# Kernel optimization log

Measured on AMD Instinct MI355X. Metric: run time of the kernel, lower is better.

## Reference

```python
import jax, jax.numpy as jnp
import numpy as np

N_NODES = 50000
N_EDGES = 800000
IN_CH = 128
MEAN_SIZE = 128
VAR_SIZE = 128


def setup_inputs() -> dict:
    key = jax.random.key(0)
    k_x, k_e, k_wm, k_wv = jax.random.split(key, 4)
    x = jax.random.normal(k_x, (N_NODES, IN_CH), dtype=jnp.float32)
    edge_index = jax.random.randint(k_e, (2, N_EDGES), 0, N_NODES, dtype=jnp.int32)
    # torch Linear(2*C, M, bias=False) weight has shape [M, 2*C]
    s = 1.0 / np.sqrt(2 * IN_CH)
    w_mean = jax.random.uniform(k_wm, (MEAN_SIZE, 2 * IN_CH), jnp.float32, -s, s)
    w_var = jax.random.uniform(k_wv, (VAR_SIZE, 2 * IN_CH), jnp.float32, -s, s)
    return {"x": x, "edge_index": edge_index, "w_mean": w_mean, "w_var": w_var}


def reference(x, edge_index, w_mean, w_var):
    row, col = edge_index[0], edge_index[1]
    x_row = x[row]  # [E, C]
    x_col = x[col]  # [E, C]
    # cat([x_row, x_col], 1) @ W.T  ==  x_row @ W[:, :C].T + x_col @ W[:, C:].T
    C = x.shape[1]
    maps_mean = jnp.einsum('ec,mc->em', x_row, w_mean[:, :C]) + \
                jnp.einsum('ec,mc->em', x_col, w_mean[:, C:])
    maps_var = jnp.einsum('ec,vc->ev', x_row, w_var[:, :C]) + \
               jnp.einsum('ec,vc->ev', x_col, w_var[:, C:])
    return (maps_mean, maps_var)
```

## Files before the change

kernel.cpp:

```cpp
#include <hip/hip_runtime.h>
#include <hip/hip_bf16.h>

#define NODES 50000
#define EDGES 800000
#define CH 128
#define NCOL 512
#define MPAD 50048
#define QROWS 64
#define EPW 4

typedef __attribute__((ext_vector_type(8))) __bf16 bf16x8;
typedef __attribute__((ext_vector_type(4))) float f32x4;
typedef __attribute__((ext_vector_type(2))) float f32x2;
typedef unsigned long long u64;

static __device__ __forceinline__ unsigned short f2bf(float f) {
    union { float f; unsigned u; } v; v.f = f;
    unsigned r = v.u + 0x7FFFu + ((v.u >> 16) & 1u);
    return (unsigned short)(r >> 16);
}

__global__ void k_cvt_x(const float* __restrict__ x, unsigned short* __restrict__ xb) {
    int i = blockIdx.x * blockDim.x + threadIdx.x;
    if (i >= MPAD * CH / 4) return;
    int base = i << 2;
    unsigned short s0 = 0, s1 = 0, s2 = 0, s3 = 0;
    if (base < NODES * CH) {
        const f32x4 v = *reinterpret_cast<const f32x4*>(x + base);
        s0 = f2bf(v[0]); s1 = f2bf(v[1]); s2 = f2bf(v[2]); s3 = f2bf(v[3]);
    }
    u64 p = (u64)s0 | ((u64)s1 << 16) | ((u64)s2 << 32) | ((u64)s3 << 48);
    *reinterpret_cast<u64*>(xb + base) = p;
}

__global__ void k_pack_w(const float* __restrict__ wm, const float* __restrict__ wv,
                         unsigned short* __restrict__ wb) {
    int i = blockIdx.x * blockDim.x + threadIdx.x;
    if (i >= NCOL * CH) return;
    int n = i >> 7, k = i & 127;
    float v;
    if (n < 128)      v = wm[n * 256 + k];
    else if (n < 256) v = wm[(n - 128) * 256 + 128 + k];
    else if (n < 384) v = wv[(n - 256) * 256 + k];
    else              v = wv[(n - 384) * 256 + 128 + k];
    wb[i] = f2bf(v);
}

__global__ __launch_bounds__(256) void k_gemmq(const unsigned short* __restrict__ xb,
                                               const unsigned short* __restrict__ wb,
                                               char* __restrict__ qt,
                                               float* __restrict__ sc) {
    __shared__ float sM[2][2][QROWS];
    __shared__ __align__(16) char sQ[QROWS][NCOL];
    const int lane = threadIdx.x & 63;
    const int wave = threadIdx.x >> 6;
    const int rowbase = blockIdx.x * QROWS;
    const int lr = lane & 15;
    const int kg = lane >> 4;

    f32x4 acc[4][8] = {};
#pragma unroll
    for (int ks = 0; ks < 4; ++ks) {
        const int k = ks * 32 + kg * 8;
        bf16x8 af[4], bfr[8];
#pragma unroll
        for (int a = 0; a < 4; ++a)
            af[a] = *reinterpret_cast<const bf16x8*>(xb + (size_t)(rowbase + a * 16 + lr) * CH + k);
#pragma unroll
        for (int b = 0; b < 8; ++b)
            bfr[b] = *reinterpret_cast<const bf16x8*>(wb + (size_t)(wave * 128 + lr * 8 + b) * CH + k);
#pragma unroll
        for (int a = 0; a < 4; ++a)
#pragma unroll
            for (int b = 0; b < 8; ++b)
                acc[a][b] = __builtin_amdgcn_mfma_f32_16x16x32_bf16(af[a], bfr[b], acc[a][b], 0, 0, 0);
    }

    const int crow = (lane >> 4) * 4;
    const int ccol = lane & 15;
    const int half = wave >> 1;

    float m[4][4];
#pragma unroll
    for (int a = 0; a < 4; ++a)
#pragma unroll
        for (int j = 0; j < 4; ++j) {
            float mm = 0.f;
#pragma unroll
            for (int b = 0; b < 8; ++b) mm = fmaxf(mm, fabsf(acc[a][b][j]));
            m[a][j] = mm;
        }
#pragma unroll
    for (int off = 1; off < 16; off <<= 1)
#pragma unroll
        for (int a = 0; a < 4; ++a)
#pragma unroll
            for (int j = 0; j < 4; ++j)
                m[a][j] = fmaxf(m[a][j], __shfl_xor(m[a][j], off, 16));
    if (ccol == 0)
#pragma unroll
        for (int a = 0; a < 4; ++a)
#pragma unroll
            for (int j = 0; j < 4; ++j)
                sM[half][wave & 1][a * 16 + crow + j] = m[a][j];
    __syncthreads();

#pragma unroll
    for (int a = 0; a < 4; ++a)
#pragma unroll
        for (int j = 0; j < 4; ++j) {
            const int row = a * 16 + crow + j;
            const float rm = fmaxf(sM[half][0][row], sM[half][1][row]);
            const float inv = (rm > 1e-20f) ? 127.0f / rm : 0.0f;
            u64 pk = 0;
#pragma unroll
            for (int b = 0; b < 8; ++b) {
                int q = __float2int_rn(acc[a][b][j] * inv);
                q = max(-127, min(127, q));
                pk |= (u64)((unsigned)q & 0xFFu) << (8 * b);
            }
            *reinterpret_cast<u64*>(&sQ[row][wave * 128 + ccol * 8]) = pk;
        }
    if (threadIdx.x < 2 * QROWS) {
        const int h = threadIdx.x >> 6, row = threadIdx.x & 63;
        const float rm = fmaxf(sM[h][0][row], sM[h][1][row]);
        sc[(size_t)(rowbase + row) * 2 + h] = (rm > 1e-20f) ? rm * (1.0f / 127.0f) : 1.0f;
    }
    __syncthreads();

#pragma unroll
    for (int t = 0; t < 8; ++t) {
        const int off = t * 4096 + threadIdx.x * 16;
        f32x4 v = *reinterpret_cast<const f32x4*>(&sQ[0][0] + off);
        *reinterpret_cast<f32x4*>(qt + (size_t)rowbase * NCOL + off) = v;
    }
}

__global__ __launch_bounds__(256) void k_edges_m(const int* __restrict__ ei,
                                                 const char* __restrict__ qt,
                                                 const float* __restrict__ sc,
                                                 float* __restrict__ out) {
    const int wave = threadIdx.x >> 6;
    const int lane = threadIdx.x & 63;
    const int es = lane >> 5;
    const int j = lane & 31;
    const int ebase = (blockIdx.x * 4 + wave) * (2 * EPW);

    int rr[EPW], cc[EPW];
#pragma unroll
    for (int i = 0; i < EPW; ++i) {
        int e = ebase + 2 * i + es;
        rr[i] = ei[e];
        cc[i] = ei[EDGES + e];
    }
    int am[EPW], av[EPW], bm[EPW], bv[EPW];
    f32x2 sr[EPW], scl[EPW];
#pragma unroll
    for (int i = 0; i < EPW; ++i) {
        const char* qr = qt + (size_t)rr[i] * NCOL;
        const char* qc = qt + (size_t)cc[i] * NCOL;
        am[i] = *reinterpret_cast<const int*>(qr + j * 4);
        av[i] = *reinterpret_cast<const int*>(qr + 256 + j * 4);
        bm[i] = *reinterpret_cast<const int*>(qc + 128 + j * 4);
        bv[i] = *reinterpret_cast<const int*>(qc + 384 + j * 4);
        sr[i]  = *reinterpret_cast<const f32x2*>(sc + (size_t)rr[i] * 2);
        scl[i] = *reinterpret_cast<const f32x2*>(sc + (size_t)cc[i] * 2);
    }
#pragma unroll
    for (int i = 0; i < EPW; ++i) {
        const int e = ebase + 2 * i + es;
        f32x4 sm_, sv_;
#pragma unroll
        for (int k = 0; k < 4; ++k) {
            const int sh = 24 - 8 * k;
            sm_[k] = sr[i][0] * (float)((am[i] << sh) >> 24)
                   + scl[i][0] * (float)((bm[i] << sh) >> 24);
            sv_[k] = sr[i][1] * (float)((av[i] << sh) >> 24)
                   + scl[i][1] * (float)((bv[i] << sh) >> 24);
        }
        __builtin_nontemporal_store(sm_,
            reinterpret_cast<f32x4*>(out + (size_t)e * 128 + j * 4));
        __builtin_nontemporal_store(sv_,
            reinterpret_cast<f32x4*>(out + (size_t)EDGES * 128 + (size_t)e * 128 + j * 4));
    }
}

__global__ void k_naive(const float* __restrict__ x, const int* __restrict__ ei,
                        const float* __restrict__ wm, const float* __restrict__ wv,
                        float* __restrict__ out) {
    __shared__ float xs[256];
    int e = blockIdx.x;
    int t = threadIdx.x;
    int r = ei[e], c = ei[EDGES + e];
    xs[t] = (t < 128) ? x[(size_t)r * 128 + t] : x[(size_t)c * 128 + (t - 128)];
    __syncthreads();
    const float* w = (t < 128) ? (wm + (size_t)t * 256) : (wv + (size_t)(t - 128) * 256);
    float acc = 0.f;
#pragma unroll 8
    for (int k = 0; k < 256; ++k) acc = fmaf(xs[k], w[k], acc);
    size_t ooff = (t < 128) ? ((size_t)e * 128 + t)
                            : ((size_t)EDGES * 128 + (size_t)e * 128 + (t - 128));
    out[ooff] = acc;
}

extern "C" void kernel_launch(void* const* d_in, const int* in_sizes, int n_in,
                              void* d_out, int out_size, void* d_ws, size_t ws_size,
                              hipStream_t stream) {
    const float* x  = (const float*)d_in[0];
    const int*   ei = (const int*)d_in[1];
    const float* wm = (const float*)d_in[2];
    const float* wv = (const float*)d_in[3];
    float* out = (float*)d_out;

    const size_t xb_b = (size_t)MPAD * CH * 2;
    const size_t wb_b = (size_t)NCOL * CH * 2;
    const size_t qt_b = (size_t)MPAD * NCOL;
    const size_t sc_b = (size_t)MPAD * 2 * 4;

    if (ws_size < xb_b + wb_b + qt_b + sc_b) {
        k_naive<<<EDGES, 256, 0, stream>>>(x, ei, wm, wv, out);
        return;
    }

    unsigned short* xb = (unsigned short*)d_ws;
    unsigned short* wb = (unsigned short*)((char*)d_ws + xb_b);
    char*           qt = (char*)d_ws + xb_b + wb_b;
    float*          sc = (float*)((char*)d_ws + xb_b + wb_b + qt_b);

    k_cvt_x<<<(MPAD * CH / 4 + 255) / 256, 256, 0, stream>>>(x, xb);
    k_pack_w<<<(NCOL * CH + 255) / 256, 256, 0, stream>>>(wm, wv, wb);
    k_gemmq<<<MPAD / QROWS, 256, 0, stream>>>(xb, wb, qt, sc);
    k_edges_m<<<EDGES / (4 * 2 * EPW), 256, 0, stream>>>(ei, qt, sc, out);
}
```

Baseline: 226.5 us.

## Group edges by source node via CSR build to reuse row projections

Builds a CSR grouping of edges by source node (histogram, single-block scan, atomic scatter) and adds an edge kernel with one wave per node. The row-side projection is loaded once per node and reused across its edges, while the column side is still gathered per edge. In exchange it adds five extra launches, a serial single-block scan, atomics, scattered output writes in nondeterministic edge order, and load imbalance from varying node degree.

```diff
diff --git a/kernel.cpp b/kernel.cpp
--- a/kernel.cpp
+++ b/kernel.cpp
@@ -136,6 +136,92 @@
     }
 }
 
+__global__ void k_zero(unsigned* __restrict__ cnt) {
+    int i = blockIdx.x * blockDim.x + threadIdx.x;
+    if (i < NODES) cnt[i] = 0;
+}
+__global__ void k_histn(const int* __restrict__ ei, unsigned* __restrict__ cnt) {
+    int e = blockIdx.x * 256 + threadIdx.x;
+    atomicAdd(&cnt[ei[e]], 1u);
+}
+__global__ __launch_bounds__(256) void k_scan(const unsigned* __restrict__ cnt,
+                                              unsigned* __restrict__ rowptr,
+                                              unsigned* __restrict__ cursor) {
+    __shared__ unsigned part[256];
+    const int t = threadIdx.x;
+    const int per = (NODES + 255) / 256;
+    const int lo = t * per, hi = min(NODES, lo + per);
+    unsigned s = 0;
+    for (int i = lo; i < hi; ++i) s += cnt[i];
+    part[t] = s;
+    __syncthreads();
+    for (int off = 1; off < 256; off <<= 1) {
+        unsigned x = (t >= off) ? part[t - off] : 0;
+        __syncthreads();
+        part[t] += x;
+        __syncthreads();
+    }
+    unsigned run = part[t] - s;
+    for (int i = lo; i < hi; ++i) { rowptr[i] = run; cursor[i] = run; run += cnt[i]; }
+}
+__global__ void k_scatter(const int* __restrict__ ei, unsigned* __restrict__ cursor,
+                          u64* __restrict__ packed) {
+    int e = blockIdx.x * 256 + threadIdx.x;
+    int r = ei[e];
+    unsigned c = (unsigned)ei[EDGES + e];
+    unsigned pos = atomicAdd(&cursor[r], 1u);
+    packed[pos] = (u64)c | ((u64)e << 32);
+}
+
+__global__ __launch_bounds__(256) void k_edges_csr(const unsigned* __restrict__ rowptr,
+                                                   const unsigned* __restrict__ cnt,
+                                                   const u64* __restrict__ packed,
+                                                   const char* __restrict__ qt,
+                                                   const float* __restrict__ sc,
+                                                   float* __restrict__ out) {
+    const int wave = threadIdx.x >> 6;
+    const int node = blockIdx.x * 4 + wave;
+    const int lane = threadIdx.x & 63;
+    const int half = lane >> 5;
+    const int j = lane & 31;
+    const unsigned start = rowptr[node];
+    const unsigned deg = cnt[node];
+    const int ar = *reinterpret_cast<const int*>(qt + (size_t)node * NCOL + half * 256 + j * 4);
+    const float s_r = sc[(size_t)node * 2 + half];
+    const size_t ob = (size_t)half * ((size_t)EDGES * 128) + (size_t)j * 4;
+
+    for (unsigned k0 = 0; k0 < deg; k0 += 4) {
+        const int n = (int)min(4u, deg - k0);
+        u64 pk[4];
+#pragma unroll
+        for (int i = 0; i < 4; ++i)
+            if (i < n) pk[i] = packed[start + k0 + i];
+        int ac[4]; float s_c[4]; unsigned ee[4];
+#pragma unroll
+        for (int i = 0; i < 4; ++i)
+            if (i < n) {
+                const unsigned c = (unsigned)(pk[i] & 0xFFFFFFFFu);
+                ee[i] = (unsigned)(pk[i] >> 32);
+                ac[i] = *reinterpret_cast<const int*>(
+                    qt + (size_t)c * NCOL + 128 + half * 256 + j * 4);
+                s_c[i] = sc[(size_t)c * 2 + half];
+            }
+#pragma unroll
+        for (int i = 0; i < 4; ++i)
+            if (i < n) {
+                f32x4 v;
+#pragma unroll
+                for (int k = 0; k < 4; ++k) {
+                    const int sh = 24 - 8 * k;
+                    v[k] = s_r * (float)((ar << sh) >> 24)
+                         + s_c[i] * (float)((ac[i] << sh) >> 24);
+                }
+                __builtin_nontemporal_store(v,
+                    reinterpret_cast<f32x4*>(out + ob + (size_t)ee[i] * 128));
+            }
+    }
+}
+
 __global__ __launch_bounds__(256) void k_edges_m(const int* __restrict__ ei,
                                                  const char* __restrict__ qt,
                                                  const float* __restrict__ sc,
@@ -145,7 +231,6 @@
     const int es = lane >> 5;
     const int j = lane & 31;
     const int ebase = (blockIdx.x * 4 + wave) * (2 * EPW);
-
     int rr[EPW], cc[EPW];
 #pragma unroll
     for (int i = 0; i < EPW; ++i) {
@@ -216,8 +301,15 @@
     const size_t wb_b = (size_t)NCOL * CH * 2;
     const size_t qt_b = (size_t)MPAD * NCOL;
     const size_t sc_b = (size_t)MPAD * 2 * 4;
-
-    if (ws_size < xb_b + wb_b + qt_b + sc_b) {
+    const size_t cnt_b = (size_t)NODES * 4;
+    const size_t rp_b  = (size_t)NODES * 4;
+    const size_t cur_b = (size_t)NODES * 4;
+    const size_t pk_b  = (size_t)EDGES * 8;
+
+    const size_t need_tab = xb_b + wb_b + qt_b + sc_b;
+    const size_t need_csr = need_tab + cnt_b + rp_b + cur_b + pk_b;
+
+    if (ws_size < need_tab) {
         k_naive<<<EDGES, 256, 0, stream>>>(x, ei, wm, wv, out);
         return;
     }
@@ -230,5 +322,18 @@
     k_cvt_x<<<(MPAD * CH / 4 + 255) / 256, 256, 0, stream>>>(x, xb);
     k_pack_w<<<(NCOL * CH + 255) / 256, 256, 0, stream>>>(wm, wv, wb);
     k_gemmq<<<MPAD / QROWS, 256, 0, stream>>>(xb, wb, qt, sc);
-    k_edges_m<<<EDGES / (4 * 2 * EPW), 256, 0, stream>>>(ei, qt, sc, out);
-}
+
+    if (ws_size >= need_csr) {
+        unsigned* cnt    = (unsigned*)((char*)d_ws + need_tab);
+        unsigned* rowptr = (unsigned*)((char*)d_ws + need_tab + cnt_b);
+        unsigned* cursor = (unsigned*)((char*)d_ws + need_tab + cnt_b + rp_b);
+        u64*      packed = (u64*)    ((char*)d_ws + need_tab + cnt_b + rp_b + cur_b);
+        k_zero<<<(NODES + 255) / 256, 256, 0, stream>>>(cnt);
+        k_histn<<<EDGES / 256, 256, 0, stream>>>(ei, cnt);
+        k_scan<<<1, 256, 0, stream>>>(cnt, rowptr, cursor);
+        k_scatter<<<EDGES / 256, 256, 0, stream>>>(ei, cursor, packed);
+        k_edges_csr<<<NODES / 4, 256, 0, stream>>>(rowptr, cnt, packed, qt, sc, out);
+    } else {
+        k_edges_m<<<EDGES / (4 * 2 * EPW), 256, 0, stream>>>(ei, qt, sc, out);
+    }
+}
```

After: 425.8 us. 1.88x slower.
